# Performance work log

Hardware: AMD Instinct MI355X
Metric: run time of the kernel (lower is better)

## Reference

```python
import jax, jax.numpy as jnp
import numpy as np

# fHOG orientation lookup (cos/sin of k*20 degrees), exactly the hardcoded
# constants used in Felzenszwalb's features.cc / mmcv extract_hog kernel.
UU = jnp.array([1.0000, 0.9397, 0.7660, 0.5000, 0.1736,
                -0.1736, -0.5000, -0.7660, -0.9397], dtype=jnp.float32)
VV = jnp.array([0.0000, 0.3420, 0.6428, 0.8660, 0.9848,
                0.9848, 0.8660, 0.6428, 0.3420], dtype=jnp.float32)
EPS = 1e-4


def _hog(img, sbin):
    B, C, H, W = img.shape
    bh = int(round(H / sbin)); bw = int(round(W / sbin))
    vh, vw = bh * sbin, bw * sbin
    # central differences at pixels (1..visible-2), source index clamped to dim-2
    ys = jnp.clip(jnp.arange(1, vh - 1), 0, H - 2)
    xs = jnp.clip(jnp.arange(1, vw - 1), 0, W - 2)
    dy = img[:, :, ys + 1][:, :, :, xs] - img[:, :, ys - 1][:, :, :, xs]
    dx = img[:, :, ys][:, :, :, xs + 1] - img[:, :, ys][:, :, :, xs - 1]
    v = dx * dx + dy * dy                      # [B,3,hg,wg]
    ch = jnp.argmax(v, axis=1, keepdims=True)  # channel with max gradient energy
    dxs = jnp.take_along_axis(dx, ch, axis=1)[:, 0]
    dys = jnp.take_along_axis(dy, ch, axis=1)[:, 0]
    mag = jnp.sqrt(dxs * dxs + dys * dys)      # [B,hg,wg]
    # snap to one of 18 signed orientations
    dot = UU[None, :, None, None] * dxs[:, None] + VV[None, :, None, None] * dys[:, None]
    best_o = jnp.argmax(jnp.concatenate([dot, -dot], axis=1), axis=1)  # [B,hg,wg]
    # bilinear spatial soft-binning into sbin x sbin cells
    yp = (jnp.arange(1, vh - 1, dtype=img.dtype) + 0.5) / sbin - 0.5
    xp = (jnp.arange(1, vw - 1, dtype=img.dtype) + 0.5) / sbin - 0.5
    iyp = jnp.floor(yp).astype(jnp.int32); ixp = jnp.floor(xp).astype(jnp.int32)
    vy0 = yp - iyp; vx0 = xp - ixp; vy1 = 1.0 - vy0; vx1 = 1.0 - vx0
    hg, wg = vh - 2, vw - 2
    bidx = jnp.arange(B)[:, None, None]
    IY = jnp.broadcast_to(iyp[None, :, None], (B, hg, wg))
    IX = jnp.broadcast_to(ixp[None, None, :], (B, hg, wg))
    WY0 = vy0[None, :, None]; WY1 = vy1[None, :, None]
    WX0 = vx0[None, None, :]; WX1 = vx1[None, None, :]
    hist = jnp.zeros((B, 18, bh, bw), dtype=img.dtype)

    def scat(h, iy, ix, w):
        valid = (iy >= 0) & (iy < bh) & (ix >= 0) & (ix < bw)
        iyc = jnp.clip(iy, 0, bh - 1); ixc = jnp.clip(ix, 0, bw - 1)
        return h.at[bidx, best_o, iyc, ixc].add(jnp.where(valid, w * mag, 0.0))

    hist = scat(hist, IY, IX, WY1 * WX1)
    hist = scat(hist, IY, IX + 1, WY1 * WX0)
    hist = scat(hist, IY + 1, IX, WY0 * WX1)
    hist = scat(hist, IY + 1, IX + 1, WY0 * WX0)
    # cell energy from contrast-insensitive sums
    s = hist[:, :9] + hist[:, 9:]
    norm = jnp.sum(s * s, axis=1)              # [B,bh,bw]
    # 2x2 block sums of norm
    T = norm[:, :-1, :-1] + norm[:, 1:, :-1] + norm[:, :-1, 1:] + norm[:, 1:, 1:]
    n1 = jax.lax.rsqrt(T[:, 1:, 1:] + EPS)[:, None]
    n2 = jax.lax.rsqrt(T[:, :-1, 1:] + EPS)[:, None]
    n3 = jax.lax.rsqrt(T[:, 1:, :-1] + EPS)[:, None]
    n4 = jax.lax.rsqrt(T[:, :-1, :-1] + EPS)[:, None]
    src = hist[:, :, 1:-1, 1:-1]               # [B,18,oh,ow]
    h1 = jnp.minimum(src * n1, 0.2); h2 = jnp.minimum(src * n2, 0.2)
    h3 = jnp.minimum(src * n3, 0.2); h4 = jnp.minimum(src * n4, 0.2)
    f_cs = 0.5 * (h1 + h2 + h3 + h4)           # 18 contrast-sensitive feats
    ss = src[:, :9] + src[:, 9:]
    f_ci = 0.5 * (jnp.minimum(ss * n1, 0.2) + jnp.minimum(ss * n2, 0.2)
                  + jnp.minimum(ss * n3, 0.2) + jnp.minimum(ss * n4, 0.2))
    tex = 0.2357 * jnp.stack([h1.sum(1), h2.sum(1), h3.sum(1), h4.sum(1)], axis=1)
    feat = jnp.concatenate([f_cs, f_ci, tex], axis=1)  # [B,31,oh,ow]
    return jnp.pad(feat, ((0, 0), (0, 0), (1, 1), (1, 1)))


def setup_inputs() -> dict:
    key = jax.random.key(0)
    img = jax.random.uniform(key, (16, 3, 512, 512), dtype=jnp.float32)
    return {"input": img, "sbin": 4}


def reference(input, sbin):
    return _hog(input, sbin)
```

## Files before the change

kernel.cpp:

```cpp
#include <hip/hip_runtime.h>
#include <hip/hip_fp16.h>

#define BATCH 16
#define H 512
#define W 512
#define BH 128
#define BW 128
#define HG 510
#define WG 510


__global__ __launch_bounds__(256, 4) void hog_gradhist(const float* __restrict__ img,
                                                       __half2* __restrict__ hist,
                                                       float* __restrict__ nrm)
{
    __shared__ unsigned int pk[68 * 72];
    __shared__ __half2 hl0[9 * 256];
    __shared__ __half2 hl1[9 * 256];

    const int t = threadIdx.x;
    const int b = blockIdx.z;
    const int cx0 = blockIdx.x * 16;
    const int cy0 = blockIdx.y * 16;
    const int gr0 = 4 * cy0 - 3;
    const int gc0 = 4 * cx0 - 4;

    const float* im = img + (size_t)b * 3 * H * W;

    const float uu[9] = {1.0f, 0.9397f, 0.766f, 0.5f, 0.1736f, -0.1736f, -0.5f, -0.766f, -0.9397f};
    const float vv[9] = {0.0f, 0.342f, 0.6428f, 0.866f, 0.9848f, 0.9848f, 0.866f, 0.6428f, 0.342f};

    const __half2 z2 = __halves2half2(__ushort_as_half(0), __ushort_as_half(0));
#pragma unroll
    for (int o = 0; o < 9; o++) { hl0[o * 256 + t] = z2; hl1[o * 256 + t] = z2; }

    for (int it = 0; it < 5; ++it) {
        int s = it * 256 + t;
        if (s >= 68 * 18) break;
        int r = s / 18;
        int q = s - r * 18;
        int gr = gr0 + r;
        int gc = gc0 + 4 * q;
        unsigned int pkv[4] = {0u, 0u, 0u, 0u};
        if (gr >= 0 && gr < HG && gc >= 0 && gc < WG) {
            int o2 = (gc == 508) ? 2 : 4;
            float bv[4] = {-1.f, -1.f, -1.f, -1.f}, bxv[4], byv[4];
            const float* p0 = im + (size_t)gr * W + gc;
#pragma unroll
            for (int c = 0; c < 3; c++) {
                const float* pu = p0 + (size_t)c * H * W;
                const float* pm = pu + W;
                const float* pd = pm + W;
                float4 a0 = *(const float4*)pu;  float2 e0 = *(const float2*)(pu + o2);
                float4 a1 = *(const float4*)pm;  float2 e1 = *(const float2*)(pm + o2);
                float4 a2 = *(const float4*)pd;  float2 e2 = *(const float2*)(pd + o2);
                float u_[6] = {a0.x, a0.y, a0.z, a0.w, e0.x, e0.y};
                float m_[6] = {a1.x, a1.y, a1.z, a1.w, e1.x, e1.y};
                float d_[6] = {a2.x, a2.y, a2.z, a2.w, e2.x, e2.y};
#pragma unroll
                for (int i = 0; i < 4; i++) {
                    float dx = __fsub_rn(m_[i + 2], m_[i]);
                    float dy = __fsub_rn(d_[i + 1], u_[i + 1]);
                    float v = __fadd_rn(__fmul_rn(dx, dx), __fmul_rn(dy, dy));
                    if (v > bv[i]) { bv[i] = v; bxv[i] = dx; byv[i] = dy; }
                }
            }
#pragma unroll
            for (int i = 0; i < 4; i++) {
                if (gc + i < WG) {
                    float mg = __fsqrt_rn(bv[i]);
                    float dt[9];
#pragma unroll
                    for (int o = 0; o < 9; o++)
                        dt[o] = __fadd_rn(__fmul_rn(uu[o], bxv[i]), __fmul_rn(vv[o], byv[i]));
                    float best = -1e30f; int bo = 0;
#pragma unroll
                    for (int o = 0; o < 9; o++) { if (dt[o] > best) { best = dt[o]; bo = o; } }
#pragma unroll
                    for (int o = 0; o < 9; o++) { float nd = -dt[o]; if (nd > best) { best = nd; bo = o + 9; } }
                    pkv[i] = (__float_as_uint(mg) & 0xFFFFFFE0u) | (unsigned int)bo;
                }
            }
        }
        *(uint4*)&pk[r * 72 + 4 * q] = make_uint4(pkv[0], pkv[1], pkv[2], pkv[3]);
    }

    __syncthreads();

    const int cxL = t & 15, cyL = t >> 4;
    const float wt8[8] = {0.125f, 0.375f, 0.625f, 0.875f, 0.875f, 0.625f, 0.375f, 0.125f};

#define ACC(B, P, WW) { unsigned _p = (P); unsigned _o = _p & 31u;                         \
        __half _hv = __float2half((WW) * __uint_as_float(_p & 0xFFFFFFE0u));               \
        bool _lo = _o < 9u; unsigned _o9 = _lo ? _o : _o - 9u;                             \
        __half2 _ad = _lo ? __halves2half2(_hv, __ushort_as_half(0))                       \
                          : __halves2half2(__ushort_as_half(0), _hv);                      \
        B[_o9 * 256 + t] = __hadd2(B[_o9 * 256 + t], _ad); }

#pragma unroll
    for (int ky = 0; ky < 8; ky++) {
        const unsigned int* row = &pk[(4 * cyL + ky) * 72];
        uint4 L = *(const uint4*)&row[4 * cxL];
        uint4 M = *(const uint4*)&row[4 * cxL + 4];
        unsigned int X = row[4 * cxL + 8];
        float wy = wt8[ky];
        ACC(hl0, L.y, wy * 0.125f);
        ACC(hl1, L.z, wy * 0.375f);
        ACC(hl0, L.w, wy * 0.625f);
        ACC(hl1, M.x, wy * 0.875f);
        ACC(hl0, M.y, wy * 0.875f);
        ACC(hl1, M.z, wy * 0.625f);
        ACC(hl0, M.w, wy * 0.375f);
        ACC(hl1, X,   wy * 0.125f);
    }
#undef ACC

    const int cx = cx0 + cxL, cy = cy0 + cyL;
    float s = 0.0f;
#pragma unroll
    for (int o = 0; o < 9; o++) {
        __half2 hh = __hadd2(hl0[o * 256 + t], hl1[o * 256 + t]);
        hist[(((size_t)b * 9 + o) * BH + cy) * BW + cx] = hh;
        float2 f = __half22float2(hh);
        float ss = f.x + f.y;
        s += ss * ss;
    }
    nrm[((size_t)b * BH + cy) * BW + cx] = s;
}

__global__ __launch_bounds__(256) void hog_feat(const __half2* __restrict__ hist,
                                                const float* __restrict__ nrm,
                                                float* __restrict__ out)
{
    int tx = threadIdx.x;
    int oy = blockIdx.y * 8 + threadIdx.y;
    int b  = blockIdx.z;
    int cx0 = tx * 4;

    if (oy == 0 || oy == BH - 1) {
        float4 z4 = make_float4(0.f, 0.f, 0.f, 0.f);
#pragma unroll
        for (int c = 0; c < 31; c++)
            *(float4*)(out + (((size_t)b * 31 + c) * BH + oy) * BW + cx0) = z4;
        return;
    }

    float v1[4], v2[4], v3[4], v4[4];
    {
        const float* nb = nrm + (size_t)b * BH * BW;
        float nn[3][6];
#pragma unroll
        for (int r = 0; r < 3; r++) {
            const float* rp = nb + (size_t)(oy - 1 + r) * BW + cx0;
#pragma unroll
            for (int j = 0; j < 6; j++) nn[r][j] = rp[j - 1];
        }
#pragma unroll
        for (int i = 0; i < 4; i++) {
            float T11 = nn[1][i+1] + nn[2][i+1] + nn[1][i+2] + nn[2][i+2];
            float T01 = nn[0][i+1] + nn[1][i+1] + nn[0][i+2] + nn[1][i+2];
            float T10 = nn[1][i]   + nn[2][i]   + nn[1][i+1] + nn[2][i+1];
            float T00 = nn[0][i]   + nn[1][i]   + nn[0][i+1] + nn[1][i+1];
            v1[i] = 1.0f / __fsqrt_rn(T11 + 1e-4f);
            v2[i] = 1.0f / __fsqrt_rn(T01 + 1e-4f);
            v3[i] = 1.0f / __fsqrt_rn(T10 + 1e-4f);
            v4[i] = 1.0f / __fsqrt_rn(T00 + 1e-4f);
        }
    }

    float h[4][18];
#pragma unroll
    for (int o = 0; o < 9; o++) {
        uint4 q = *(const uint4*)(hist + (((size_t)b * 9 + o) * BH + oy) * BW + cx0);
        unsigned vs[4] = {q.x, q.y, q.z, q.w};
#pragma unroll
        for (int i = 0; i < 4; i++) {
            float2 f = __half22float2(*(__half2*)&vs[i]);
            h[i][o] = f.x; h[i][o + 9] = f.y;
        }
    }

    bool msk[4];
#pragma unroll
    for (int i = 0; i < 4; i++) { int cxi = cx0 + i; msk[i] = (cxi >= 1 && cxi <= 126); }

    float t1[4] = {0,0,0,0}, t2[4] = {0,0,0,0}, t3[4] = {0,0,0,0}, t4[4] = {0,0,0,0};
    float* ob = out + ((size_t)b * 31) * BH * BW + (size_t)oy * BW + cx0;

#pragma unroll
    for (int o = 0; o < 18; o++) {
        float st[4];
#pragma unroll
        for (int i = 0; i < 4; i++) {
            float s = h[i][o];
            float a1 = fminf(s * v1[i], 0.2f);
            float a2 = fminf(s * v2[i], 0.2f);
            float a3 = fminf(s * v3[i], 0.2f);
            float a4 = fminf(s * v4[i], 0.2f);
            t1[i] += a1; t2[i] += a2; t3[i] += a3; t4[i] += a4;
            st[i] = msk[i] ? 0.5f * (a1 + a2 + a3 + a4) : 0.f;
        }
        *(float4*)(ob + (size_t)o * BH * BW) = make_float4(st[0], st[1], st[2], st[3]);
    }
#pragma unroll
    for (int o = 0; o < 9; o++) {
        float st[4];
#pragma unroll
        for (int i = 0; i < 4; i++) {
            float ss = h[i][o] + h[i][o + 9];
            float a1 = fminf(ss * v1[i], 0.2f);
            float a2 = fminf(ss * v2[i], 0.2f);
            float a3 = fminf(ss * v3[i], 0.2f);
            float a4 = fminf(ss * v4[i], 0.2f);
            st[i] = msk[i] ? 0.5f * (a1 + a2 + a3 + a4) : 0.f;
        }
        *(float4*)(ob + (size_t)(18 + o) * BH * BW) = make_float4(st[0], st[1], st[2], st[3]);
    }
    {
        float s1[4], s2[4], s3[4], s4[4];
#pragma unroll
        for (int i = 0; i < 4; i++) {
            s1[i] = msk[i] ? 0.2357f * t1[i] : 0.f;
            s2[i] = msk[i] ? 0.2357f * t2[i] : 0.f;
            s3[i] = msk[i] ? 0.2357f * t3[i] : 0.f;
            s4[i] = msk[i] ? 0.2357f * t4[i] : 0.f;
        }
        *(float4*)(ob + (size_t)27 * BH * BW) = make_float4(s1[0], s1[1], s1[2], s1[3]);
        *(float4*)(ob + (size_t)28 * BH * BW) = make_float4(s2[0], s2[1], s2[2], s2[3]);
        *(float4*)(ob + (size_t)29 * BH * BW) = make_float4(s3[0], s3[1], s3[2], s3[3]);
        *(float4*)(ob + (size_t)30 * BH * BW) = make_float4(s4[0], s4[1], s4[2], s4[3]);
    }
}

extern "C" void kernel_launch(void* const* d_in, const int* in_sizes, int n_in,
                              void* d_out, int out_size, void* d_ws, size_t ws_size,
                              hipStream_t stream)
{
    const float* img = (const float*)d_in[0];
    float* out = (float*)d_out;
    char* ws = (char*)d_ws;

    __half2* hist = (__half2*)ws;
    float* nrm    = (float*)(ws + 9437184);

    dim3 b1(256, 1, 1), g1(BW / 16, BH / 16, BATCH);
    hog_gradhist<<<g1, b1, 0, stream>>>(img, hist, nrm);

    dim3 b3(32, 8, 1), g3(1, BH / 8, BATCH);
    hog_feat<<<g3, b3, 0, stream>>>(hist, nrm, out);
}
```

Measured before the change: 121.5 us.

## Compute 4x4 gradient pixels per thread to reuse row loads; pad shared stride

Each thread now computes a 4x4 block of gradient pixels, loading a 6-row window per channel once instead of 3 rows per single output row. This cuts the global load count per pixel from 3 rows to 1.5 rows. The shared-memory row stride changes from 72 to 76, probably to reduce bank conflicts. In exchange, register pressure rises (16-element arrays plus a 6x6 window) under launch bounds of 4 blocks per CU, and only 306 of 256x2 thread slots do work, so the loop is less balanced.

```diff
diff --git a/kernel.cpp b/kernel.cpp
--- a/kernel.cpp
+++ b/kernel.cpp
@@ -8,13 +8,14 @@
 #define BW 128
 #define HG 510
 #define WG 510
+#define PKS 76
 
 
 __global__ __launch_bounds__(256, 4) void hog_gradhist(const float* __restrict__ img,
                                                        __half2* __restrict__ hist,
                                                        float* __restrict__ nrm)
 {
-    __shared__ unsigned int pk[68 * 72];
+    __shared__ unsigned int pk[68 * PKS];
     __shared__ __half2 hl0[9 * 256];
     __shared__ __half2 hl1[9 * 256];
 
@@ -34,55 +35,71 @@
 #pragma unroll
     for (int o = 0; o < 9; o++) { hl0[o * 256 + t] = z2; hl1[o * 256 + t] = z2; }
 
-    for (int it = 0; it < 5; ++it) {
-        int s = it * 256 + t;
-        if (s >= 68 * 18) break;
-        int r = s / 18;
-        int q = s - r * 18;
-        int gr = gr0 + r;
+    for (int it = 0; it < 2; ++it) {
+        int u = it * 256 + t;
+        if (u >= 17 * 18) break;
+        int R = u / 18;
+        int q = u - R * 18;
+        int gr = gr0 + 4 * R;
         int gc = gc0 + 4 * q;
-        unsigned int pkv[4] = {0u, 0u, 0u, 0u};
-        if (gr >= 0 && gr < HG && gc >= 0 && gc < WG) {
+        unsigned pkq[4][4] = {{0u,0u,0u,0u},{0u,0u,0u,0u},{0u,0u,0u,0u},{0u,0u,0u,0u}};
+        if (gc >= 0 && gc < WG) {
             int o2 = (gc == 508) ? 2 : 4;
-            float bv[4] = {-1.f, -1.f, -1.f, -1.f}, bxv[4], byv[4];
-            const float* p0 = im + (size_t)gr * W + gc;
+            float bv[16], bxv[16], byv[16];
+#pragma unroll
+            for (int k = 0; k < 16; k++) { bv[k] = -1.f; bxv[k] = 0.f; byv[k] = 0.f; }
 #pragma unroll
             for (int c = 0; c < 3; c++) {
-                const float* pu = p0 + (size_t)c * H * W;
-                const float* pm = pu + W;
-                const float* pd = pm + W;
-                float4 a0 = *(const float4*)pu;  float2 e0 = *(const float2*)(pu + o2);
-                float4 a1 = *(const float4*)pm;  float2 e1 = *(const float2*)(pm + o2);
-                float4 a2 = *(const float4*)pd;  float2 e2 = *(const float2*)(pd + o2);
-                float u_[6] = {a0.x, a0.y, a0.z, a0.w, e0.x, e0.y};
-                float m_[6] = {a1.x, a1.y, a1.z, a1.w, e1.x, e1.y};
-                float d_[6] = {a2.x, a2.y, a2.z, a2.w, e2.x, e2.y};
-#pragma unroll
-                for (int i = 0; i < 4; i++) {
-                    float dx = __fsub_rn(m_[i + 2], m_[i]);
-                    float dy = __fsub_rn(d_[i + 1], u_[i + 1]);
-                    float v = __fadd_rn(__fmul_rn(dx, dx), __fmul_rn(dy, dy));
-                    if (v > bv[i]) { bv[i] = v; bxv[i] = dx; byv[i] = dy; }
+                const float* base = im + (size_t)c * H * W;
+                float Wr[6][6];
+#pragma unroll
+                for (int k = 0; k < 6; k++) {
+                    int pr = gr + k;
+                    pr = (pr < 0) ? 0 : (pr > 511 ? 511 : pr);
+                    const float* rowp = base + (size_t)pr * W + gc;
+                    float4 a = *(const float4*)rowp;
+                    float2 e = *(const float2*)(rowp + o2);
+                    Wr[k][0] = a.x; Wr[k][1] = a.y; Wr[k][2] = a.z; Wr[k][3] = a.w;
+                    Wr[k][4] = e.x; Wr[k][5] = e.y;
+                }
+#pragma unroll
+                for (int r = 0; r < 4; r++) {
+#pragma unroll
+                    for (int i = 0; i < 4; i++) {
+                        float dx = __fsub_rn(Wr[r + 1][i + 2], Wr[r + 1][i]);
+                        float dy = __fsub_rn(Wr[r + 2][i + 1], Wr[r][i + 1]);
+                        float v = __fadd_rn(__fmul_rn(dx, dx), __fmul_rn(dy, dy));
+                        int k = r * 4 + i;
+                        if (v > bv[k]) { bv[k] = v; bxv[k] = dx; byv[k] = dy; }
+                    }
                 }
             }
 #pragma unroll
-            for (int i = 0; i < 4; i++) {
-                if (gc + i < WG) {
-                    float mg = __fsqrt_rn(bv[i]);
-                    float dt[9];
-#pragma unroll
-                    for (int o = 0; o < 9; o++)
-                        dt[o] = __fadd_rn(__fmul_rn(uu[o], bxv[i]), __fmul_rn(vv[o], byv[i]));
-                    float best = -1e30f; int bo = 0;
-#pragma unroll
-                    for (int o = 0; o < 9; o++) { if (dt[o] > best) { best = dt[o]; bo = o; } }
-#pragma unroll
-                    for (int o = 0; o < 9; o++) { float nd = -dt[o]; if (nd > best) { best = nd; bo = o + 9; } }
-                    pkv[i] = (__float_as_uint(mg) & 0xFFFFFFE0u) | (unsigned int)bo;
+            for (int j = 0; j < 4; j++) {
+                if ((unsigned)(gr + j) < (unsigned)HG) {
+#pragma unroll
+                    for (int i = 0; i < 4; i++) {
+                        if (gc + i < WG) {
+                            int k = j * 4 + i;
+                            float mg = __fsqrt_rn(bv[k]);
+                            float dt[9];
+#pragma unroll
+                            for (int o = 0; o < 9; o++)
+                                dt[o] = __fadd_rn(__fmul_rn(uu[o], bxv[k]), __fmul_rn(vv[o], byv[k]));
+                            float best = -1e30f; int bo = 0;
+#pragma unroll
+                            for (int o = 0; o < 9; o++) { if (dt[o] > best) { best = dt[o]; bo = o; } }
+#pragma unroll
+                            for (int o = 0; o < 9; o++) { float nd = -dt[o]; if (nd > best) { best = nd; bo = o + 9; } }
+                            pkq[j][i] = (__float_as_uint(mg) & 0xFFFFFFE0u) | (unsigned int)bo;
+                        }
+                    }
                 }
             }
         }
-        *(uint4*)&pk[r * 72 + 4 * q] = make_uint4(pkv[0], pkv[1], pkv[2], pkv[3]);
+#pragma unroll
+        for (int j = 0; j < 4; j++)
+            *(uint4*)&pk[(4 * R + j) * PKS + 4 * q] = make_uint4(pkq[j][0], pkq[j][1], pkq[j][2], pkq[j][3]);
     }
 
     __syncthreads();
@@ -99,7 +116,7 @@
 
 #pragma unroll
     for (int ky = 0; ky < 8; ky++) {
-        const unsigned int* row = &pk[(4 * cyL + ky) * 72];
+        const unsigned int* row = &pk[(4 * cyL + ky) * PKS];
         uint4 L = *(const uint4*)&row[4 * cxL];
         uint4 M = *(const uint4*)&row[4 * cxL + 4];
         unsigned int X = row[4 * cxL + 8];
```

After: 129.4 us. 6.5% more time.
